# Optimization experiments

Hardware: AMD Instinct MI355X
Metric: run time of the kernel (lower is better)

## Reference

```python
import jax, jax.numpy as jnp
import numpy as np

B, C, E, HLR, WLR = 2, 64, 4, 192, 192


def setup_inputs() -> dict:
    key = jax.random.key(0)
    ks = jax.random.split(key, 8)
    s = 0.05  # keep activations/offsets in a sane range
    return {
        "x": jax.random.normal(ks[0], (B, C, HLR, WLR), jnp.float32),
        "fused": jax.random.normal(ks[1], (B, C, HLR, WLR), jnp.float32),
        "weight_compress": jax.random.normal(ks[2], (E, C // 8, C), jnp.float32) * s,
        "weight_expand": jax.random.normal(ks[3], (E, C, C // 8), jnp.float32) * s,
        "body_w1": jax.random.normal(ks[4], (64, 4), jnp.float32) * s,
        "body_b1": jnp.zeros((64,), jnp.float32),
        "body_w2": jax.random.normal(ks[5], (64, 64), jnp.float32) * s,
        "body_b2": jnp.zeros((64,), jnp.float32),
        "routing_w": jax.random.normal(ks[6], (E, 64), jnp.float32) * s,
        "routing_b": jnp.zeros((E,), jnp.float32),
        "offset_w": jax.random.normal(ks[7], (2, 64), jnp.float32) * s,
        "offset_b": jnp.zeros((2,), jnp.float32),
        "scale": 2,
    }


def _conv1x1(x, w, b):
    # x: [n, cin, H, W], w: [cout, cin] (1x1 conv)
    return jnp.einsum('oc,nchw->nohw', w, x) + b[None, :, None, None]


def _grid_sample(img, px, py):
    # Bilinear sample, align_corners=True semantics, zeros padding.
    # img: [b,c,h,w]; px, py: [b,H,W] absolute LR pixel coords.
    b, c, h, w = img.shape
    x0 = jnp.floor(px)
    y0 = jnp.floor(py)
    wx = (px - x0)[:, None]  # [b,1,H,W]
    wy = (py - y0)[:, None]

    def gather(xi, yi):
        valid = (xi >= 0) & (xi <= w - 1) & (yi >= 0) & (yi <= h - 1)
        xc = jnp.clip(xi, 0, w - 1).astype(jnp.int32)
        yc = jnp.clip(yi, 0, h - 1).astype(jnp.int32)
        v = jax.vmap(lambda im, yy, xx: im[:, yy, xx])(img, yc, xc)  # [b,c,H,W]
        return v * valid[:, None].astype(img.dtype)

    v00 = gather(x0, y0)
    v01 = gather(x0 + 1, y0)
    v10 = gather(x0, y0 + 1)
    v11 = gather(x0 + 1, y0 + 1)
    top = v00 * (1 - wx) + v01 * wx
    bot = v10 * (1 - wx) + v11 * wx
    return top * (1 - wy) + bot * wy


def reference(x, fused, weight_compress, weight_expand, body_w1, body_b1,
              body_w2, body_b2, routing_w, routing_b, offset_w, offset_b, scale):
    b, c, h, w = fused.shape
    H, W = round(h * scale), round(w * scale)
    e, c8 = weight_compress.shape[0], weight_compress.shape[1]

    ch = jnp.arange(H, dtype=jnp.float32)
    cw = jnp.arange(W, dtype=jnp.float32)
    coor_h = (ch + 0.5) / scale - jnp.floor((ch + 0.5) / scale + 0.001) - 0.5  # [H]
    coor_w = (cw + 0.5) / scale - jnp.floor((cw + 0.5) / scale + 0.001) - 0.5  # [W]
    inp = jnp.stack([
        jnp.full((H, W), 1.0 / scale, jnp.float32),
        jnp.full((H, W), 1.0 / scale, jnp.float32),
        jnp.broadcast_to(coor_h[:, None], (H, W)),
        jnp.broadcast_to(coor_w[None, :], (H, W)),
    ], 0)[None]  # [1,4,H,W]

    emb = jax.nn.relu(_conv1x1(inp, body_w1, body_b1))
    emb = jax.nn.relu(_conv1x1(emb, body_w2, body_b2))
    offset = _conv1x1(emb, offset_w, offset_b)            # [1,2,H,W]
    routing = jax.nn.sigmoid(_conv1x1(emb, routing_w, routing_b))  # [1,E,H,W]

    rw = routing.reshape(e, H * W).T                      # [HW, E]
    wc = (rw @ weight_compress.reshape(e, -1)).reshape(H, W, c8, c)  # per-pixel compress
    we = (rw @ weight_expand.reshape(e, -1)).reshape(H, W, c, c8)    # per-pixel expand

    # deformable sample: HR grid projected into LR space + learned offset (pixel units)
    px = jnp.broadcast_to((cw[None, :] + 0.5) / scale - 0.5, (H, W))[None] + offset[:, 0]
    py = jnp.broadcast_to((ch[:, None] + 0.5) / scale - 0.5, (H, W))[None] + offset[:, 1]
    px = jnp.broadcast_to(px, (b, H, W))
    py = jnp.broadcast_to(py, (b, H, W))
    fea0 = _grid_sample(fused, px, py)                    # [b,c,H,W]

    fea = fea0.transpose(0, 2, 3, 1)                      # [b,H,W,c]
    mid = jnp.einsum('hwoc,bhwc->bhwo', wc, fea)          # [b,H,W,c//8]
    out = jnp.einsum('hwco,bhwo->bhwc', we, mid)          # [b,H,W,c]
    return out.transpose(0, 3, 1, 2) + fea0
```

## Files before the change

### kernel.cpp

```cpp
#include <hip/hip_runtime.h>
#include <hip/hip_fp16.h>
#include <math.h>

typedef __attribute__((ext_vector_type(8))) _Float16 half8;
typedef __attribute__((ext_vector_type(4))) float f32x4;

#define HLR_ 192
#define WLR_ 192
#define H_ 384
#define W_ 384
#define LRP (HLR_*WLR_)
#define PTILES (LRP/64)
#define TPX 96
#define NTW (W_/TPX)
#define IPW 48
#define RUN 6

#define WS_K_OFF 2359296
#define WS_OFF_OFF (WS_K_OFF + 8192)

__device__ __forceinline__ unsigned short f32_f16(float x){
    union { _Float16 h; unsigned short u; } c; c.h = (_Float16)x; return c.u;
}
__device__ __forceinline__ unsigned int pk_f16(float a, float b){
    union { _Float16 h[2]; unsigned int u; } c;
    c.h[0] = (_Float16)a; c.h[1] = (_Float16)b; return c.u;
}
__device__ __forceinline__ half8 splat8(float f){
    _Float16 h = (_Float16)f;
    half8 v = {h,h,h,h,h,h,h,h};
    return v;
}

__global__ __launch_bounds__(256) void prep_kernel(
    const float* __restrict__ fused, unsigned short* __restrict__ fused_t,
    const float* __restrict__ w1, const float* __restrict__ b1,
    const float* __restrict__ w2, const float* __restrict__ b2,
    const float* __restrict__ rw, const float* __restrict__ rb,
    const float* __restrict__ ow, const float* __restrict__ ob,
    const float* __restrict__ WC, const float* __restrict__ WE,
    unsigned short* __restrict__ Kmat, float* __restrict__ g_off)
{
    __shared__ float smem[8912];
    int bid = blockIdx.x;
    int tid = threadIdx.x;

    if (bid == 0) {
        float* sW2 = smem;
        float* sRW = smem + 4160;
        float* sE1 = smem + 4544;
        float* sR  = smem + 4800;
        float* sWc = smem + 4816;
        float* sWe = smem + 6864;

        for (int idx = tid; idx < 4096; idx += 256)
            sW2[(idx>>6)*65 + (idx&63)] = w2[idx];
        sRW[tid] = rw[tid];
        if (tid < 128) sRW[256 + tid] = ow[tid];

        int wave = tid >> 6, lane = tid & 63;
        int ph = wave >> 1, pw = wave & 1;

        float ch = (ph + 0.5f)*0.5f;
        float coor_h = ch - floorf(ch + 0.001f) - 0.5f;
        float cw = (pw + 0.5f)*0.5f;
        float coor_w = cw - floorf(cw + 0.001f) - 0.5f;

        float e1 = w1[lane*4+0]*0.5f + w1[lane*4+1]*0.5f
                 + w1[lane*4+2]*coor_h + w1[lane*4+3]*coor_w + b1[lane];
        sE1[wave*64 + lane] = fmaxf(e1, 0.0f);
        __syncthreads();

        float e2 = b2[lane];
        #pragma unroll 16
        for (int i = 0; i < 64; ++i) e2 += sW2[lane*65 + i] * sE1[wave*64 + i];
        e2 = fmaxf(e2, 0.0f);

        #pragma unroll
        for (int k = 0; k < 6; ++k) {
            float t = sRW[k*64 + lane] * e2;
            #pragma unroll
            for (int m = 1; m <= 32; m <<= 1) t += __shfl_xor(t, m, 64);
            if (lane == 0) {
                if (k < 4) sR[wave*4 + k] = 1.0f/(1.0f + expf(-(t + rb[k])));
                else       g_off[wave*2 + (k-4)] = t + ob[k-4];
            }
        }
        __syncthreads();

        for (int idx = tid; idx < 2048; idx += 256) {
            int cls = idx >> 9, rem = idx & 511;
            float r0=sR[cls*4+0], r1=sR[cls*4+1], r2=sR[cls*4+2], r3=sR[cls*4+3];
            sWc[cls*512 + rem] =
                r0*WC[0*512+rem] + r1*WC[1*512+rem] + r2*WC[2*512+rem] + r3*WC[3*512+rem];
        }
        for (int idx = tid; idx < 2048; idx += 256) {
            int cls = idx >> 9, rem = idx & 511;
            float r0=sR[cls*4+0], r1=sR[cls*4+1], r2=sR[cls*4+2], r3=sR[cls*4+3];
            sWe[cls*512 + rem] =
                r0*WE[0*512+rem] + r1*WE[1*512+rem] + r2*WE[2*512+rem] + r3*WE[3*512+rem];
        }
        __syncthreads();

        for (int idx = tid; idx < 16384; idx += 256) {
            int cls = idx >> 12, rem = idx & 4095;
            int c = rem >> 6, cp = rem & 63;
            float a = (c == cp) ? 1.0f : 0.0f;
            #pragma unroll
            for (int o = 0; o < 8; ++o)
                a += sWe[cls*512 + c*8 + o] * sWc[cls*512 + o*64 + cp];
            Kmat[idx] = f32_f16(a);
        }
    } else {
        float* tile = smem;
        int id = bid - 1;
        int b = id / PTILES, pt = id % PTILES;
        int p0 = pt * 64;
        #pragma unroll
        for (int i = 0; i < 4; ++i) {
            int n = tid + i*256;
            int c = n >> 4, k = (n & 15) << 2;
            f32x4 v = *(const f32x4*)(fused + (size_t)(b*64 + c)*LRP + p0 + k);
            float* tp = tile + c*65 + k;
            tp[0]=v[0]; tp[1]=v[1]; tp[2]=v[2]; tp[3]=v[3];
        }
        __syncthreads();
        int c0 = (tid & 15) << 2, pr = tid >> 4;
        #pragma unroll
        for (int i = 0; i < 4; ++i) {
            int p = pr + i*16;
            uint2 pv;
            pv.x = pk_f16(tile[(c0+0)*65 + p], tile[(c0+1)*65 + p]);
            pv.y = pk_f16(tile[(c0+2)*65 + p], tile[(c0+3)*65 + p]);
            *(uint2*)(fused_t + (((size_t)(b*LRP + p0 + p)) << 6) + c0) = pv;
        }
    }
}

__global__ __launch_bounds__(256, 6) void main_kernel(
    const unsigned short* __restrict__ fused_t, const unsigned short* __restrict__ Kmat,
    const float* __restrict__ g_off, float* __restrict__ out)
{
    __shared__ unsigned short sFea[4*IPW*64];

    int g = blockIdx.x;
    int xcd = g & 7;
    int t = g >> 3;
    int q = t >> 2;
    int wt = t & 3;
    int h = xcd*48 + q;
    int w0 = wt * TPX;
    int tid = threadIdx.x, wave = tid >> 6, lane = tid & 63;
    int b = wave >> 1, par = wave & 1;
    int ph = h & 1, cls = ph*2 + par;

    float off0 = g_off[cls*2 + 0];
    float off1 = g_off[cls*2 + 1];

    float py  = (h + 0.5f)*0.5f - 0.5f + off1;
    float y0f = floorf(py);
    float wy  = py - y0f;
    int   y0  = (int)y0f;
    float fy0 = (y0 >= 0  && y0 <= HLR_-1) ? 1.0f : 0.0f;
    float fy1 = (y0 >= -1 && y0 <= HLR_-2) ? 1.0f : 0.0f;
    int   yc0 = min(max(y0, 0), HLR_-1);
    int   yc1 = min(max(y0+1, 0), HLR_-1);
    float omwy = 1.0f - wy;

    float pxb  = (w0 + par + 0.5f)*0.5f - 0.5f + off0;
    float x0bf = floorf(pxb);
    float wx   = pxb - x0bf;
    int   x0b  = (int)x0bf;
    float omwx = 1.0f - wx;

    float W00 = omwx*omwy*fy0, W01 = wx*omwy*fy0;
    float W10 = omwx*wy  *fy1, W11 = wx*wy  *fy1;

    int itg = lane >> 3;
    int cg  = lane & 7;

    const unsigned short* baseB = fused_t + (size_t)b * LRP * 64;
    const unsigned short* r0 = baseB + (size_t)yc0 * WLR_ * 64 + cg*8;
    const unsigned short* r1 = baseB + (size_t)yc1 * WLR_ * 64 + cg*8;
    unsigned short* sW = sFea + wave*IPW*64;

    int xs = x0b + itg*RUN;
    int xc = min(max(xs, 0), WLR_-1);
    half8 p0 = *(const half8*)(r0 + (size_t)xc*64);
    half8 p1 = *(const half8*)(r1 + (size_t)xc*64);
    float fxp = (xs >= 0 && xs <= WLR_-1) ? 1.0f : 0.0f;

    #pragma unroll
    for (int j = 0; j < RUN; ++j) {
        int xn = xs + j + 1;
        float fxn = (xn >= 0 && xn <= WLR_-1) ? 1.0f : 0.0f;
        int xcn = min(max(xn, 0), WLR_-1);
        half8 c0 = *(const half8*)(r0 + (size_t)xcn*64);
        half8 c1 = *(const half8*)(r1 + (size_t)xcn*64);
        half8 v = p0*splat8(W00*fxp);
        v += c0*splat8(W01*fxn);
        v += p1*splat8(W10*fxp);
        v += c1*splat8(W11*fxn);
        int item = itg*RUN + j;
        *(half8*)(sW + (item << 6) + ((cg ^ (item & 7)) << 3)) = v;
        p0 = c0; p1 = c1; fxp = fxn;
    }
    __syncthreads();

    int lm = lane & 15, lg = lane >> 4;

    const unsigned short* Kc = Kmat + cls*4096;
    half8 Af[4][2];
    #pragma unroll
    for (int mt = 0; mt < 4; ++mt)
        #pragma unroll
        for (int kt = 0; kt < 2; ++kt)
            Af[mt][kt] = *(const half8*)(Kc + (mt*16 + lm)*64 + kt*32 + lg*8);

    #pragma unroll
    for (int nt = 0; nt < 3; ++nt) {
        int slot = nt*16 + lm;
        const unsigned short* sb = sFea + (wave*IPW + slot)*64;
        half8 B0 = *(const half8*)(sb + (((0*4 + lg) ^ (slot & 7)) << 3));
        half8 B1 = *(const half8*)(sb + (((1*4 + lg) ^ (slot & 7)) << 3));

        int wc = w0 + 2*slot + par;
        #pragma unroll
        for (int mt = 0; mt < 4; ++mt) {
            f32x4 a = {0.0f, 0.0f, 0.0f, 0.0f};
            a = __builtin_amdgcn_mfma_f32_16x16x32_f16(Af[mt][0], B0, a, 0, 0, 0);
            a = __builtin_amdgcn_mfma_f32_16x16x32_f16(Af[mt][1], B1, a, 0, 0, 0);
            int c0r = mt*16 + lg*4;
            float* op = out + (((size_t)(b*64 + c0r)*H_ + h)*W_ + wc);
            op[0*(size_t)(H_*W_)] = a[0];
            op[1*(size_t)(H_*W_)] = a[1];
            op[2*(size_t)(H_*W_)] = a[2];
            op[3*(size_t)(H_*W_)] = a[3];
        }
    }
}

extern "C" void kernel_launch(void* const* d_in, const int* in_sizes, int n_in,
                              void* d_out, int out_size, void* d_ws, size_t ws_size,
                              hipStream_t stream)
{
    const float* fused = (const float*)d_in[1];
    const float* WC    = (const float*)d_in[2];
    const float* WE    = (const float*)d_in[3];
    const float* w1    = (const float*)d_in[4];
    const float* b1    = (const float*)d_in[5];
    const float* w2    = (const float*)d_in[6];
    const float* b2    = (const float*)d_in[7];
    const float* rw    = (const float*)d_in[8];
    const float* rb    = (const float*)d_in[9];
    const float* ow    = (const float*)d_in[10];
    const float* ob    = (const float*)d_in[11];
    (void)in_sizes; (void)n_in; (void)out_size; (void)ws_size;

    float* ws = (float*)d_ws;
    unsigned short* fused_t = (unsigned short*)ws;
    unsigned short* Kmat = (unsigned short*)(ws + WS_K_OFF);
    float* g_off = ws + WS_OFF_OFF;
    float* o = (float*)d_out;

    hipLaunchKernelGGL(prep_kernel, dim3(1 + 2*PTILES), dim3(256), 0, stream,
                       fused, fused_t, w1, b1, w2, b2, rw, rb, ow, ob, WC, WE,
                       Kmat, g_off);
    hipLaunchKernelGGL(main_kernel, dim3(H_*NTW), dim3(256), 0, stream,
                       fused_t, Kmat, g_off, o);
}
```

Baseline: 144.0 us.

## Fuse fp16 transpose of fused into main kernel via per-wave LR row buffer

```diff
diff --git a/kernel.cpp b/kernel.cpp
--- a/kernel.cpp
+++ b/kernel.cpp
@@ -10,14 +10,12 @@
 #define H_ 384
 #define W_ 384
 #define LRP (HLR_*WLR_)
-#define PTILES (LRP/64)
 #define TPX 96
 #define NTW (W_/TPX)
 #define IPW 48
-#define RUN 6
-
-#define WS_K_OFF 2359296
-#define WS_OFF_OFF (WS_K_OFF + 8192)
+#define NCOL 52
+
+#define WS_OFF_OFF 8192
 
 __device__ __forceinline__ unsigned short f32_f16(float x){
     union { _Float16 h; unsigned short u; } c; c.h = (_Float16)x; return c.u;
@@ -26,14 +24,12 @@
     union { _Float16 h[2]; unsigned int u; } c;
     c.h[0] = (_Float16)a; c.h[1] = (_Float16)b; return c.u;
 }
-__device__ __forceinline__ half8 splat8(float f){
-    _Float16 h = (_Float16)f;
+__device__ __forceinline__ half8 splat8h(_Float16 h){
     half8 v = {h,h,h,h,h,h,h,h};
     return v;
 }
 
 __global__ __launch_bounds__(256) void prep_kernel(
-    const float* __restrict__ fused, unsigned short* __restrict__ fused_t,
     const float* __restrict__ w1, const float* __restrict__ b1,
     const float* __restrict__ w2, const float* __restrict__ b2,
     const float* __restrict__ rw, const float* __restrict__ rb,
@@ -42,106 +38,80 @@
     unsigned short* __restrict__ Kmat, float* __restrict__ g_off)
 {
     __shared__ float smem[8912];
-    int bid = blockIdx.x;
     int tid = threadIdx.x;
 
-    if (bid == 0) {
-        float* sW2 = smem;
-        float* sRW = smem + 4160;
-        float* sE1 = smem + 4544;
-        float* sR  = smem + 4800;
-        float* sWc = smem + 4816;
-        float* sWe = smem + 6864;
-
-        for (int idx = tid; idx < 4096; idx += 256)
-            sW2[(idx>>6)*65 + (idx&63)] = w2[idx];
-        sRW[tid] = rw[tid];
-        if (tid < 128) sRW[256 + tid] = ow[tid];
-
-        int wave = tid >> 6, lane = tid & 63;
-        int ph = wave >> 1, pw = wave & 1;
-
-        float ch = (ph + 0.5f)*0.5f;
-        float coor_h = ch - floorf(ch + 0.001f) - 0.5f;
-        float cw = (pw + 0.5f)*0.5f;
-        float coor_w = cw - floorf(cw + 0.001f) - 0.5f;
-
-        float e1 = w1[lane*4+0]*0.5f + w1[lane*4+1]*0.5f
-                 + w1[lane*4+2]*coor_h + w1[lane*4+3]*coor_w + b1[lane];
-        sE1[wave*64 + lane] = fmaxf(e1, 0.0f);
-        __syncthreads();
-
-        float e2 = b2[lane];
-        #pragma unroll 16
-        for (int i = 0; i < 64; ++i) e2 += sW2[lane*65 + i] * sE1[wave*64 + i];
-        e2 = fmaxf(e2, 0.0f);
-
-        #pragma unroll
-        for (int k = 0; k < 6; ++k) {
-            float t = sRW[k*64 + lane] * e2;
-            #pragma unroll
-            for (int m = 1; m <= 32; m <<= 1) t += __shfl_xor(t, m, 64);
-            if (lane == 0) {
-                if (k < 4) sR[wave*4 + k] = 1.0f/(1.0f + expf(-(t + rb[k])));
-                else       g_off[wave*2 + (k-4)] = t + ob[k-4];
-            }
+    float* sW2 = smem;
+    float* sRW = smem + 4160;
+    float* sE1 = smem + 4544;
+    float* sR  = smem + 4800;
+    float* sWc = smem + 4816;
+    float* sWe = smem + 6864;
+
+    for (int idx = tid; idx < 4096; idx += 256)
+        sW2[(idx>>6)*65 + (idx&63)] = w2[idx];
+    sRW[tid] = rw[tid];
+    if (tid < 128) sRW[256 + tid] = ow[tid];
+
+    int wave = tid >> 6, lane = tid & 63;
+    int ph = wave >> 1, pw = wave & 1;
+
+    float ch = (ph + 0.5f)*0.5f;
+    float coor_h = ch - floorf(ch + 0.001f) - 0.5f;
+    float cw = (pw + 0.5f)*0.5f;
+    float coor_w = cw - floorf(cw + 0.001f) - 0.5f;
+
+    float e1 = w1[lane*4+0]*0.5f + w1[lane*4+1]*0.5f
+             + w1[lane*4+2]*coor_h + w1[lane*4+3]*coor_w + b1[lane];
+    sE1[wave*64 + lane] = fmaxf(e1, 0.0f);
+    __syncthreads();
+
+    float e2 = b2[lane];
+    #pragma unroll 16
+    for (int i = 0; i < 64; ++i) e2 += sW2[lane*65 + i] * sE1[wave*64 + i];
+    e2 = fmaxf(e2, 0.0f);
+
+    #pragma unroll
+    for (int k = 0; k < 6; ++k) {
+        float t = sRW[k*64 + lane] * e2;
+        #pragma unroll
+        for (int m = 1; m <= 32; m <<= 1) t += __shfl_xor(t, m, 64);
+        if (lane == 0) {
+            if (k < 4) sR[wave*4 + k] = 1.0f/(1.0f + expf(-(t + rb[k])));
+            else       g_off[wave*2 + (k-4)] = t + ob[k-4];
         }
-        __syncthreads();
-
-        for (int idx = tid; idx < 2048; idx += 256) {
-            int cls = idx >> 9, rem = idx & 511;
-            float r0=sR[cls*4+0], r1=sR[cls*4+1], r2=sR[cls*4+2], r3=sR[cls*4+3];
-            sWc[cls*512 + rem] =
-                r0*WC[0*512+rem] + r1*WC[1*512+rem] + r2*WC[2*512+rem] + r3*WC[3*512+rem];
-        }
-        for (int idx = tid; idx < 2048; idx += 256) {
-            int cls = idx >> 9, rem = idx & 511;
-            float r0=sR[cls*4+0], r1=sR[cls*4+1], r2=sR[cls*4+2], r3=sR[cls*4+3];
-            sWe[cls*512 + rem] =
-                r0*WE[0*512+rem] + r1*WE[1*512+rem] + r2*WE[2*512+rem] + r3*WE[3*512+rem];
-        }
-        __syncthreads();
-
-        for (int idx = tid; idx < 16384; idx += 256) {
-            int cls = idx >> 12, rem = idx & 4095;
-            int c = rem >> 6, cp = rem & 63;
-            float a = (c == cp) ? 1.0f : 0.0f;
-            #pragma unroll
-            for (int o = 0; o < 8; ++o)
-                a += sWe[cls*512 + c*8 + o] * sWc[cls*512 + o*64 + cp];
-            Kmat[idx] = f32_f16(a);
-        }
-    } else {
-        float* tile = smem;
-        int id = bid - 1;
-        int b = id / PTILES, pt = id % PTILES;
-        int p0 = pt * 64;
-        #pragma unroll
-        for (int i = 0; i < 4; ++i) {
-            int n = tid + i*256;
-            int c = n >> 4, k = (n & 15) << 2;
-            f32x4 v = *(const f32x4*)(fused + (size_t)(b*64 + c)*LRP + p0 + k);
-            float* tp = tile + c*65 + k;
-            tp[0]=v[0]; tp[1]=v[1]; tp[2]=v[2]; tp[3]=v[3];
-        }
-        __syncthreads();
-        int c0 = (tid & 15) << 2, pr = tid >> 4;
-        #pragma unroll
-        for (int i = 0; i < 4; ++i) {
-            int p = pr + i*16;
-            uint2 pv;
-            pv.x = pk_f16(tile[(c0+0)*65 + p], tile[(c0+1)*65 + p]);
-            pv.y = pk_f16(tile[(c0+2)*65 + p], tile[(c0+3)*65 + p]);
-            *(uint2*)(fused_t + (((size_t)(b*LRP + p0 + p)) << 6) + c0) = pv;
-        }
+    }
+    __syncthreads();
+
+    for (int idx = tid; idx < 2048; idx += 256) {
+        int cls = idx >> 9, rem = idx & 511;
+        float r0=sR[cls*4+0], r1=sR[cls*4+1], r2=sR[cls*4+2], r3=sR[cls*4+3];
+        sWc[cls*512 + rem] =
+            r0*WC[0*512+rem] + r1*WC[1*512+rem] + r2*WC[2*512+rem] + r3*WC[3*512+rem];
+    }
+    for (int idx = tid; idx < 2048; idx += 256) {
+        int cls = idx >> 9, rem = idx & 511;
+        float r0=sR[cls*4+0], r1=sR[cls*4+1], r2=sR[cls*4+2], r3=sR[cls*4+3];
+        sWe[cls*512 + rem] =
+            r0*WE[0*512+rem] + r1*WE[1*512+rem] + r2*WE[2*512+rem] + r3*WE[3*512+rem];
+    }
+    __syncthreads();
+
+    for (int idx = tid; idx < 16384; idx += 256) {
+        int cls = idx >> 12, rem = idx & 4095;
+        int c = rem >> 6, cp = rem & 63;
+        float a = (c == cp) ? 1.0f : 0.0f;
+        #pragma unroll
+        for (int o = 0; o < 8; ++o)
+            a += sWe[cls*512 + c*8 + o] * sWc[cls*512 + o*64 + cp];
+        Kmat[idx] = f32_f16(a);
     }
 }
 
 __global__ __launch_bounds__(256, 6) void main_kernel(
-    const unsigned short* __restrict__ fused_t, const unsigned short* __restrict__ Kmat,
+    const float* __restrict__ fused, const unsigned short* __restrict__ Kmat,
     const float* __restrict__ g_off, float* __restrict__ out)
 {
-    __shared__ unsigned short sFea[4*IPW*64];
+    __shared__ unsigned short rowbuf[4*NCOL*64];
 
     int g = blockIdx.x;
     int xcd = g & 7;
@@ -165,7 +135,8 @@
     float fy1 = (y0 >= -1 && y0 <= HLR_-2) ? 1.0f : 0.0f;
     int   yc0 = min(max(y0, 0), HLR_-1);
     int   yc1 = min(max(y0+1, 0), HLR_-1);
-    float omwy = 1.0f - wy;
+    float A0 = (1.0f - wy)*fy0;
+    float A1 = wy*fy1;
 
     float pxb  = (w0 + par + 0.5f)*0.5f - 0.5f + off0;
     float x0bf = floorf(pxb);
@@ -173,37 +144,47 @@
     int   x0b  = (int)x0bf;
     float omwx = 1.0f - wx;
 
-    float W00 = omwx*omwy*fy0, W01 = wx*omwy*fy0;
-    float W10 = omwx*wy  *fy1, W11 = wx*wy  *fy1;
-
-    int itg = lane >> 3;
-    int cg  = lane & 7;
-
-    const unsigned short* baseB = fused_t + (size_t)b * LRP * 64;
-    const unsigned short* r0 = baseB + (size_t)yc0 * WLR_ * 64 + cg*8;
-    const unsigned short* r1 = baseB + (size_t)yc1 * WLR_ * 64 + cg*8;
-    unsigned short* sW = sFea + wave*IPW*64;
-
-    int xs = x0b + itg*RUN;
-    int xc = min(max(xs, 0), WLR_-1);
-    half8 p0 = *(const half8*)(r0 + (size_t)xc*64);
-    half8 p1 = *(const half8*)(r1 + (size_t)xc*64);
-    float fxp = (xs >= 0 && xs <= WLR_-1) ? 1.0f : 0.0f;
-
-    #pragma unroll
-    for (int j = 0; j < RUN; ++j) {
-        int xn = xs + j + 1;
-        float fxn = (xn >= 0 && xn <= WLR_-1) ? 1.0f : 0.0f;
-        int xcn = min(max(xn, 0), WLR_-1);
-        half8 c0 = *(const half8*)(r0 + (size_t)xcn*64);
-        half8 c1 = *(const half8*)(r1 + (size_t)xcn*64);
-        half8 v = p0*splat8(W00*fxp);
-        v += c0*splat8(W01*fxn);
-        v += p1*splat8(W10*fxp);
-        v += c1*splat8(W11*fxn);
-        int item = itg*RUN + j;
-        *(half8*)(sW + (item << 6) + ((cg ^ (item & 7)) << 3)) = v;
-        p0 = c0; p1 = c1; fxp = fxn;
+    int xbase = min(max(x0b, 0), WLR_-51);
+    int dx = x0b - xbase;
+
+    unsigned short* rw_base = rowbuf + wave*(NCOL*64);
+
+    int cq  = lane >> 4;
+    int xch = lane & 15;
+    int x3  = xch & 3;
+    if (xch < 13) {
+        int xs_g = xbase + 4*xch;
+        #pragma unroll 2
+        for (int k = 0; k < 8; ++k) {
+            int kk = (k + x3) & 7;
+            int c0 = cq*16 + 2*kk;
+            const float* p00 = fused + ((size_t)(b*64 + c0)*HLR_ + yc0)*WLR_ + xs_g;
+            const float* p01 = fused + ((size_t)(b*64 + c0)*HLR_ + yc1)*WLR_ + xs_g;
+            const float* p10 = p00 + LRP;
+            const float* p11 = p01 + LRP;
+            f32x4 a0, a1, b0, b1;
+            if (xs_g <= WLR_-4) {
+                a0 = *(const f32x4*)p00; a1 = *(const f32x4*)p01;
+                b0 = *(const f32x4*)p10; b1 = *(const f32x4*)p11;
+            } else {
+                #pragma unroll
+                for (int j = 0; j < 4; ++j) {
+                    int xj = min(xs_g + j, WLR_-1) - xs_g;
+                    a0[j] = p00[xj]; a1[j] = p01[xj];
+                    b0[j] = p10[xj]; b1[j] = p11[xj];
+                }
+            }
+            f32x4 e = a0*A0 + a1*A1;
+            f32x4 f = b0*A0 + b1*A1;
+            int chb = c0 >> 3, coff = c0 & 7;
+            #pragma unroll
+            for (int j = 0; j < 4; ++j) {
+                int col = 4*xch + j;
+                int chunk = chb ^ (col & 7);
+                *(unsigned int*)(rw_base + col*64 + (chunk<<3) + coff) =
+                    pk_f16(e[j], f[j]);
+            }
+        }
     }
     __syncthreads();
 
@@ -220,9 +201,20 @@
     #pragma unroll
     for (int nt = 0; nt < 3; ++nt) {
         int slot = nt*16 + lm;
-        const unsigned short* sb = sFea + (wave*IPW + slot)*64;
-        half8 B0 = *(const half8*)(sb + (((0*4 + lg) ^ (slot & 7)) << 3));
-        half8 B1 = *(const half8*)(sb + (((1*4 + lg) ^ (slot & 7)) << 3));
+        int x_s = x0b + slot;
+        float fxp = (x_s >= 0  && x_s <= WLR_-1) ? 1.0f : 0.0f;
+        float fxn = (x_s >= -1 && x_s <= WLR_-2) ? 1.0f : 0.0f;
+        int col  = min(max(slot + dx,     0), NCOL-1);
+        int col1 = min(max(slot + 1 + dx, 0), NCOL-1);
+        _Float16 W0 = (_Float16)(omwx * fxp);
+        _Float16 W1 = (_Float16)(wx   * fxn);
+
+        half8 P00 = *(const half8*)(rw_base + col *64 + (((0+lg) ^ (col &7))<<3));
+        half8 P01 = *(const half8*)(rw_base + col1*64 + (((0+lg) ^ (col1&7))<<3));
+        half8 P10 = *(const half8*)(rw_base + col *64 + (((4+lg) ^ (col &7))<<3));
+        half8 P11 = *(const half8*)(rw_base + col1*64 + (((4+lg) ^ (col1&7))<<3));
+        half8 B0 = P00*splat8h(W0) + P01*splat8h(W1);
+        half8 B1 = P10*splat8h(W0) + P11*splat8h(W1);
 
         int wc = w0 + 2*slot + par;
         #pragma unroll
@@ -258,14 +250,12 @@
     (void)in_sizes; (void)n_in; (void)out_size; (void)ws_size;
 
     float* ws = (float*)d_ws;
-    unsigned short* fused_t = (unsigned short*)ws;
-    unsigned short* Kmat = (unsigned short*)(ws + WS_K_OFF);
+    unsigned short* Kmat = (unsigned short*)ws;
     float* g_off = ws + WS_OFF_OFF;
     float* o = (float*)d_out;
 
-    hipLaunchKernelGGL(prep_kernel, dim3(1 + 2*PTILES), dim3(256), 0, stream,
-                       fused, fused_t, w1, b1, w2, b2, rw, rb, ow, ob, WC, WE,
-                       Kmat, g_off);
+    hipLaunchKernelGGL(prep_kernel, dim3(1), dim3(256), 0, stream,
+                       w1, b1, w2, b2, rw, rb, ow, ob, WC, WE, Kmat, g_off);
     hipLaunchKernelGGL(main_kernel, dim3(H_*NTW), dim3(256), 0, stream,
-                       fused_t, Kmat, g_off, o);
-}
+                       fused, Kmat, g_off, o);
+}
```

Result: slower. 164.9 us (+14.5%).
